# Optimization experiments

Hardware: AMD Instinct MI355X
Metric: run time of the kernel (lower is better)

The kernel has to match this reference:

```python
import jax, jax.numpy as jnp
import numpy as np

B, H, W = 4, 256, 256
TARGET_BETA0 = 5
TARGET_LIFETIME = 0.5
LOSS_SCALE = 100.0


def setup_inputs() -> dict:
    key = jax.random.key(0)
    k1, k2 = jax.random.split(key)
    prob_map = jax.random.uniform(k1, (B, 1, H, W), dtype=jnp.float32)
    roi_mask = (jax.random.uniform(k2, (B, 1, H, W)) < 0.9).astype(jnp.float32)
    return {"prob_map": prob_map, "roi_mask": roi_mask}


def _ph0_topk_loss(f):
    """0-dim persistent homology (V-filtration, 4-connectivity) of f:[H,W],
    then standard top-k MSE(target_lifetime) loss. Equivalent to
    cripser.compute_ph_torch(f, maxdim=0, filtration='V') + _standard_loss.
    Algorithm: Kruskal over grid edges with weight max(f[u],f[v]), elder rule.
    All combinatorics run on stop_gradient values; births/deaths are
    differentiable gathers from f at the paired pixel indices."""
    Hh, Ww = f.shape
    N = Hh * Ww
    fv = f.reshape(-1)
    fvc = jax.lax.stop_gradient(fv)

    idx2d = jnp.arange(N, dtype=jnp.int32).reshape(Hh, Ww)
    r_u = idx2d[:, :-1].reshape(-1)  # right edges
    r_v = r_u + 1
    d_u = idx2d[:-1, :].reshape(-1)  # down edges
    d_v = d_u + Ww
    eu = jnp.concatenate([r_u, d_u])
    ev = jnp.concatenate([r_v, d_v])
    ew = jnp.maximum(fvc[eu], fvc[ev])
    order = jnp.argsort(ew)  # process edges by increasing filtration value
    eu, ev = eu[order], ev[order]

    parent0 = jnp.arange(N, dtype=jnp.int32)

    def step(parent, uv):
        u, v = uv[0], uv[1]

        def find(x):
            return jax.lax.while_loop(lambda y: parent[y] != y, lambda y: parent[y], x)

        ru = find(u)
        rv = find(v)
        merge = ru != rv
        # Invariant: a root is the argmin pixel of its component, so
        # fvc[root] is the component's birth value. Elder rule: the root
        # with smaller birth value survives (ties -> smaller index).
        older_u = (fvc[ru] < fvc[rv]) | ((fvc[ru] == fvc[rv]) & (ru < rv))
        keep = jnp.where(older_u, ru, rv)
        die = jnp.where(older_u, rv, ru)
        b_idx = jnp.where(merge, die, -1)  # birth pixel of the dying comp
        d_pix = jnp.where(fvc[u] >= fvc[v], u, v)  # death = max endpoint
        d_idx = jnp.where(merge, d_pix, -1)
        parent = parent.at[die].set(jnp.where(merge, keep, die))
        parent = parent.at[u].set(jnp.where(merge, keep, ru))  # path compression
        parent = parent.at[v].set(jnp.where(merge, keep, rv))
        return parent, (b_idx, d_idx)

    _, (pb, pd_) = jax.lax.scan(step, parent0, jnp.stack([eu, ev], axis=1))

    valid = pb >= 0
    births = fv[jnp.maximum(pb, 0)]
    deaths = fv[jnp.maximum(pd_, 0)]
    life = jnp.where(valid, deaths - births, 0.0)  # lifetimes >= 0

    # sort descending; invalid slots to the end (keys are stop-gradient)
    key_ = jnp.where(valid, jax.lax.stop_gradient(life), -jnp.inf)
    top = jnp.argsort(-key_)[:TARGET_BETA0]
    topk = life[top]
    vk = valid[top]
    n_use = jnp.sum(vk)  # = min(num_finite, target_beta0)
    sq = jnp.where(vk, (topk - TARGET_LIFETIME) ** 2, 0.0)
    return jnp.sum(sq) / jnp.maximum(n_use, 1).astype(f.dtype)


def reference(prob_map, roi_mask):
    prob = prob_map[:, 0] * roi_mask[:, 0]  # roi masking; (1-roi)*0 is a no-op
    filtration = 1.0 - prob
    losses = jax.vmap(_ph0_topk_loss)(filtration)
    return jnp.mean(losses) * LOSS_SCALE
```

## Files before the change

kernel.cpp:

```cpp
#include <hip/hip_runtime.h>
#include <stdint.h>

#define NPIX 65536
#define NRE  65280
#define NE   130560
#define NIMG 4
#define LTPB 1024
#define ETPB 1024
#define NBLK_L (NIMG*32)
#define TPIX 2048
#define EPAD 4096
#define KMAX 4096
#define HSZ  1024
#define LHSZ 2048
#define ECAP 4096
typedef unsigned long long u64;

__device__ __forceinline__ int ufind(unsigned* lbl, int x){
  int r = x, c = (int)lbl[r];
  while (c != r){ r = c; c = (int)lbl[r]; }
  while ((int)lbl[x] != r){ int n = (int)lbl[x]; lbl[x] = (unsigned)r; x = n; }
  return r;
}
__device__ __forceinline__ int ufind16(unsigned short* uf, int x){
  int r = x, c = (int)uf[r];
  while (c != r){ r = c; c = (int)uf[r]; }
  while ((int)uf[x] != r){ int n = (int)uf[x]; uf[x] = (unsigned short)r; x = n; }
  return r;
}

__device__ __forceinline__ void merge5(float* a, const float* b){
  float out[5]; int ia = 0, ib = 0;
  #pragma unroll
  for (int k = 0; k < 5; ++k){
    float av = (ia < 5) ? a[ia] : -2.0f;
    float bv = (ib < 5) ? b[ib] : -2.0f;
    if (av >= bv){ out[k] = av; ++ia; } else { out[k] = bv; ++ib; }
  }
  #pragma unroll
  for (int k = 0; k < 5; ++k) a[k] = out[k];
}

__device__ __forceinline__ void ins5(float* t5, float v){
  if (v > t5[4]){
    int j = 4;
    while (j > 0 && t5[j-1] < v){ t5[j] = t5[j-1]; --j; }
    t5[j] = v;
  }
}

__global__ __launch_bounds__(LTPB)
void ph0_local(const float* __restrict__ prob, const float* __restrict__ roi,
               float* __restrict__ Fg, float* __restrict__ LIFEg,
               unsigned* __restrict__ LBLg, u64* __restrict__ LAg,
               unsigned* __restrict__ C, unsigned* __restrict__ C2,
               unsigned* __restrict__ MAPg, unsigned* __restrict__ KGg,
               float* __restrict__ T5g)
{
  const int blk = blockIdx.x;
  const int img = blk >> 5;
  const int tile = blk & 31;
  const int tr = tile >> 2, tc = tile & 3;
  const int gr0 = tr*32, gc0 = tc*64;
  const int tid = threadIdx.x;
  const int lane = tid & 63;

  const float* pm = prob + img*NPIX;
  const float* rm = roi  + img*NPIX;
  float* F = Fg + img*NPIX;
  float* LIFE = LIFEg + img*NPIX;
  unsigned* LBL = LBLg + img*NPIX;
  unsigned* MAP = MAPg + img*NPIX;
  unsigned* KG  = KGg  + img*NPIX;
  u64* LA = LAg + (size_t)img*NE;

  __shared__ float          sf[TPIX];
  __shared__ unsigned       slbl[TPIX];
  __shared__ unsigned       smeb[2][TPIX];
  __shared__ unsigned short el[2][EPAD];
  __shared__ unsigned       aux[EPAD];
  __shared__ unsigned       bkw[192];
  __shared__ unsigned short bkp[192];
  __shared__ unsigned       s_fired[TPIX/32];
  __shared__ float          s_t5w[(LTPB/64)*5];
  __shared__ int s_n[3];

  float t5[5] = {-1.f,-1.f,-1.f,-1.f,-1.f};

  for (int p = tid; p < TPIX; p += LTPB){
    int gp = ((gr0 + (p>>6))<<8) + gc0 + (p&63);
    float fv = 1.0f - pm[gp]*rm[gp];
    sf[p] = fv; slbl[p] = (unsigned)p;
    smeb[0][p] = 0xFFFFFFFFu; smeb[1][p] = 0xFFFFFFFFu;
    F[gp] = fv; LIFE[gp] = 0.0f;
  }
  if (tid < 3) s_n[tid] = 0;
  if (tid < TPIX/32) s_fired[tid] = 0;
  for (int s = tid; s < 192; s += LTPB){
    unsigned wv = 0xFFFFFFFFu; int p = 0; int gq = -1;
    if (s < 32){ if (tc > 0){ p = s*64;        gq = ((gr0+s)<<8)    + gc0 - 1;  } }
    else if (s < 64){ int k=s-32;  if (tc < 3){ p = k*64+63;  gq = ((gr0+k)<<8)  + gc0 + 64; } }
    else if (s < 128){ int k=s-64; if (tr > 0){ p = k;        gq = ((gr0-1)<<8)  + gc0 + k;  } }
    else { int k=s-128;            if (tr < 7){ p = 31*64+k;  gq = ((gr0+32)<<8) + gc0 + k;  } }
    if (gq >= 0){
      int gp = ((gr0 + (p>>6))<<8) + gc0 + (p&63);
      float fp = 1.0f - pm[gp]*rm[gp];
      float fq = 1.0f - pm[gq]*rm[gq];
      wv = __float_as_uint(fmaxf(fp, fq));
    }
    bkw[s] = wv; bkp[s] = (unsigned short)p;
  }
  __syncthreads();

  int M = EPAD, cur = 0;
  for (int rd = 0; rd < 100000; ++rd){
    int nxt = cur ^ 1;
    unsigned* sme = smeb[rd & 1];
    if (tid < 192){
      unsigned wv = bkw[tid];
      if (wv != 0xFFFFFFFFu) atomicMin(&sme[ufind(slbl, (int)bkp[tid])], wv);
    }
    int Mpad = (M + 63) & ~63;
    for (int idx = tid; idx < Mpad; idx += LTPB){
      bool keep = false; int e=0,u=0,v=0,a=0,b=0;
      if (idx < M){
        e = (rd == 0) ? idx : (int)el[cur][idx];
        bool valid;
        if (e < 2048){ u=e; v=e+1; valid = ((e&63)!=63); }
        else { u=e-2048; v=u+64; valid = ((u>>6)!=31); }
        if (valid){
          a = ufind(slbl,u); b = ufind(slbl,v);
          if (a != b){
            unsigned wb = __float_as_uint(fmaxf(sf[u],sf[v]));
            atomicMin(&sme[a],wb); atomicMin(&sme[b],wb);
            keep = true;
          }
        }
      }
      u64 m = __ballot(keep);
      if (m){
        int pos0 = __popcll(m & ((1ULL<<lane)-1));
        int leader = __ffsll((long long)m)-1;
        int base = 0;
        if (lane == leader) base = atomicAdd(&s_n[rd%3], __popcll(m));
        base = __shfl(base, leader);
        if (keep){
          el[nxt][base+pos0] = (unsigned short)e;
          aux[base+pos0] = (unsigned)a | ((unsigned)b<<16);
        }
      }
    }
    __syncthreads();
    int n = s_n[rd%3];
    cur = nxt;
    if (n == M || n == 0){ M = n; break; }
    M = n;
    for (int idx = tid; idx < M; idx += LTPB){
      int e = (int)el[cur][idx];
      unsigned ab = aux[idx];
      int a = (int)(ab & 0xFFFFu), b = (int)(ab >> 16);
      int u, v;
      if (e < 2048){ u = e; v = e + 1; } else { u = e - 2048; v = u + 64; }
      float w = fmaxf(sf[u], sf[v]);
      unsigned wb = __float_as_uint(w);
      float fa = sf[a], fb = sf[b];
      bool bd = (fb < fa) || ((fb == fa) && (b < a));
      int die = bd ? a : b, keep = bd ? b : a;
      if (sme[die] == wb){
        slbl[die] = (unsigned)keep;
        int gd = ((gr0 + (die>>6))<<8) + gc0 + (die&63);
        float lt = w - (bd ? fa : fb);
        LIFE[gd] = lt;
        unsigned bbit = 1u << (die & 31);
        if (!(atomicOr(&s_fired[die >> 5], bbit) & bbit)) ins5(t5, lt);
      }
    }
    {
      unsigned* smeN = smeb[(rd+1) & 1];
      for (int i = tid; i < TPIX; i += LTPB) smeN[i] = 0xFFFFFFFFu;
      if (tid == 0) s_n[(rd+1)%3] = 0;
    }
    __syncthreads();
  }

  unsigned* posm = smeb[0];
  for (int p = tid; p < TPIX; p += LTPB){
    int r = ufind(slbl, p);
    int gp = ((gr0 + (p>>6))<<8) + gc0 + (p&63);
    LBL[gp] = (unsigned)(((gr0 + (r>>6))<<8) + gc0 + (r&63));
  }
  __syncthreads();
  for (int p = tid; p < TPIX; p += LTPB){
    if ((int)slbl[p] == p){
      unsigned pos = atomicAdd(&C2[img], 1u);
      posm[p] = pos;
      unsigned gp = (unsigned)(((gr0 + (p>>6))<<8) + gc0 + (p&63));
      MAP[gp] = pos;
      KG[pos] = gp;
    }
  }
  __syncthreads();

  unsigned* hk = (unsigned*)&el[cur ^ 1][0];
  unsigned* hw = slbl;
  for (int i = tid; i < LHSZ; i += LTPB){ hk[i] = 0xFFFFFFFFu; hw[i] = 0xFFFFFFFFu; }
  __syncthreads();

  unsigned* ctr = &C[img];
  int Mpad2 = (M + 63) & ~63;
  for (int idx = tid; idx < Mpad2; idx += LTPB){
    bool spill = false;
    u64 rec = 0;
    if (idx < M){
      int e = (int)el[cur][idx];
      unsigned ab = aux[idx];
      int a = (int)(ab & 0xFFFFu), b = (int)(ab >> 16);
      int u, v;
      if (e < 2048){ u = e; v = e + 1; } else { u = e - 2048; v = u + 64; }
      unsigned wb = __float_as_uint(fmaxf(sf[u], sf[v]));
      int lo = a < b ? a : b, hi = a < b ? b : a;
      unsigned key = ((unsigned)lo << 11) | (unsigned)hi;
      unsigned h = ((key * 2654435761u) >> 21) & (LHSZ-1);
      bool ins = false;
      #pragma unroll
      for (int t = 0; t < 8; ++t){
        unsigned old = atomicCAS(&hk[h], 0xFFFFFFFFu, key);
        if (old == 0xFFFFFFFFu || old == key){ atomicMin(&hw[h], wb); ins = true; break; }
        h = (h + 1) & (LHSZ-1);
      }
      if (!ins){
        spill = true;
        rec = ((u64)wb << 32) | ((u64)posm[a] << 16) | posm[b];
      }
    }
    u64 m = __ballot(spill);
    if (m){
      int pos0 = __popcll(m & ((1ULL<<lane)-1));
      int leader = __ffsll((long long)m)-1;
      unsigned base = 0;
      if (lane == leader) base = atomicAdd(ctr, (unsigned)__popcll(m));
      base = (unsigned)__shfl((int)base, leader);
      if (spill) LA[base + pos0] = rec;
    }
  }
  __syncthreads();
  for (int h = tid; h < LHSZ; h += LTPB){
    unsigned key = hk[h];
    bool ok = (key != 0xFFFFFFFFu);
    u64 rec = 0;
    if (ok){
      int a = (int)(key >> 11), b = (int)(key & 0x7FFu);
      rec = ((u64)hw[h] << 32) | ((u64)posm[a] << 16) | posm[b];
    }
    u64 m = __ballot(ok);
    if (m){
      int pos0 = __popcll(m & ((1ULL<<lane)-1));
      int leader = __ffsll((long long)m)-1;
      unsigned base = 0;
      if (lane == leader) base = atomicAdd(ctr, (unsigned)__popcll(m));
      base = (unsigned)__shfl((int)base, leader);
      if (ok) LA[base + pos0] = rec;
    }
  }

  #pragma unroll
  for (int off = 1; off < 64; off <<= 1){
    float o[5];
    #pragma unroll
    for (int k = 0; k < 5; ++k) o[k] = __shfl_xor(t5[k], off);
    merge5(t5, o);
  }
  if (lane == 0){
    int wv = tid >> 6;
    #pragma unroll
    for (int k = 0; k < 5; ++k) s_t5w[wv*5+k] = t5[k];
  }
  __syncthreads();
  if (tid < 64){
    float u5[5];
    #pragma unroll
    for (int k = 0; k < 5; ++k) u5[k] = (tid < LTPB/64) ? s_t5w[tid*5+k] : -2.0f;
    #pragma unroll
    for (int off = 1; off < 16; off <<= 1){
      float o[5];
      #pragma unroll
      for (int k = 0; k < 5; ++k) o[k] = __shfl_xor(u5[k], off);
      merge5(u5, o);
    }
    if (tid == 0){
      #pragma unroll
      for (int k = 0; k < 5; ++k) T5g[blk*5+k] = u5[k];
    }
  }
}

#define RUN_ROUNDS_GLOBAL(UF, ME, RNK)                                       \
  for (int k = tid; k < K; k += ETPB){                                       \
    unsigned g = kg[k];                                                      \
    UF[k] = (unsigned short)k;                                               \
    RNK[k] = ((u64)__float_as_uint(f[g]) << 32) | g;                         \
  }                                                                          \
  __syncthreads();                                                           \
  for (int rd = 0; rd < 70000 && n > 0; ++rd){                               \
    for (int k = tid; k < K; k += ETPB) ME[k] = 0xFFFFFFFFu;                 \
    if (tid == 0) s_n[0] = 0;                                                \
    __syncthreads();                                                         \
    int Mpad = (n + 63) & ~63;                                               \
    for (int idx = tid; idx < Mpad; idx += ETPB){                            \
      bool keep = false; unsigned wb = 0; int a = 0, b = 0;                  \
      if (idx < n){                                                          \
        u64 rec = src[idx];                                                  \
        wb = (unsigned)(rec >> 32);                                          \
        a = (int)((rec >> 16) & 0xFFFFu);                                    \
        b = (int)(rec & 0xFFFFu);                                            \
        a = ufind16(UF, a); b = ufind16(UF, b);                              \
        if (a != b){ atomicMin(&ME[a], wb); atomicMin(&ME[b], wb); keep = true; } \
      }                                                                      \
      u64 m = __ballot(keep);                                                \
      if (m){                                                                \
        int pos0 = __popcll(m & ((1ULL<<lane)-1));                           \
        int leader = __ffsll((long long)m)-1;                                \
        int base = 0;                                                        \
        if (lane == leader) base = atomicAdd(&s_n[0], __popcll(m));          \
        base = __shfl(base, leader);                                         \
        if (keep) dst[base+pos0] = ((u64)wb<<32)|((u64)(unsigned)a<<16)|(unsigned)b; \
      }                                                                      \
    }                                                                        \
    __syncthreads();                                                         \
    int nn = s_n[0];                                                         \
    for (int idx = tid; idx < nn; idx += ETPB){                              \
      u64 rec = dst[idx];                                                    \
      unsigned wb = (unsigned)(rec >> 32);                                   \
      int a = (int)((rec >> 16) & 0xFFFFu);                                  \
      int b = (int)(rec & 0xFFFFu);                                          \
      bool bd = RNK[b] < RNK[a];                                             \
      int die = bd ? a : b, kp = bd ? b : a;                                 \
      if (ME[die] == wb){                                                    \
        UF[die] = (unsigned short)kp;                                        \
        u64 rk = RNK[die];                                                   \
        life[(unsigned)(rk & 0xFFFFFFFFu)] =                                 \
            __uint_as_float(wb) - __uint_as_float((unsigned)(rk >> 32));     \
      }                                                                      \
    }                                                                        \
    __syncthreads();                                                         \
    u64* t = src; src = dst; dst = t; n = nn;                                \
  }

__global__ __launch_bounds__(ETPB)
void ph0_endgame(const float* __restrict__ Fg, float* __restrict__ LIFEg,
                 unsigned* __restrict__ LBLg, unsigned* __restrict__ MAPg,
                 unsigned* __restrict__ KGg, u64* __restrict__ LAg,
                 u64* __restrict__ LBg, u64* __restrict__ GRg,
                 const unsigned* __restrict__ C, const unsigned* __restrict__ C2,
                 const float* __restrict__ T5g,
                 float* __restrict__ LOSS, unsigned* __restrict__ DONE,
                 float* __restrict__ out)
{
  const int img = blockIdx.x, tid = threadIdx.x;
  const int lane = tid & 63;
  const float* f = Fg + img*NPIX;
  float* life = LIFEg + img*NPIX;
  unsigned* lblg = LBLg + img*NPIX;
  unsigned* map  = MAPg + img*NPIX;
  const unsigned* kg = KGg + img*NPIX;
  u64* src = LAg + (size_t)img*NE;
  u64* dst = LBg + (size_t)img*NE;
  u64* rnk = GRg + (size_t)img*NPIX;

  __shared__ unsigned short s_uf[KMAX];
  __shared__ unsigned s_meB[2*KMAX];
  __shared__ unsigned s_hkB[2*HSZ];
  __shared__ unsigned s_hwB[2*HSZ];
  __shared__ u64 s_rnk[KMAX];
  __shared__ u64 s_lstA[ECAP];
  __shared__ u64 s_lstB[ECAP];
  __shared__ unsigned s_fired[KMAX/32];
  __shared__ float s_w5[(ETPB/64)*5];
  __shared__ int s_n[3];

  const int K = (int)C2[img];
  const int nInt = (int)C[img];

  for (int s = tid; s < 2560; s += ETPB){
    int gu, gv;
    if (s < 768){ int ci = s >> 8, row = s & 255, col = 63 + (ci<<6); gu = (row<<8)+col; gv = gu+1; }
    else { int k = s - 768; int ri = k >> 8, colh = k & 255, gr = 31 + (ri<<5); gu = (gr<<8)+colh; gv = gu+256; }
    unsigned ia = map[lblg[gu]];
    unsigned ib = map[lblg[gv]];
    unsigned wb = __float_as_uint(fmaxf(f[gu], f[gv]));
    src[nInt + s] = ((u64)wb << 32) | ((u64)ia << 16) | ib;
  }
  if (tid < 3) s_n[tid] = 0;
  int n = nInt + 2560;

  float t5[5] = {-1.f,-1.f,-1.f,-1.f,-1.f};

  if (K <= KMAX){
    for (int k = tid; k < K; k += ETPB){
      unsigned g = kg[k];
      s_uf[k] = (unsigned short)k;
      s_rnk[k] = ((u64)__float_as_uint(f[g]) << 32) | g;
      s_meB[k] = 0xFFFFFFFFu;
    }
    for (int h = tid; h < HSZ; h += ETPB){ s_hkB[h] = 0xFFFFFFFFu; s_hwB[h] = 0xFFFFFFFFu; }
    if (tid < KMAX/32) s_fired[tid] = 0;
    if (tid < 32*5) ins5(t5, T5g[img*(32*5) + tid]);
    __syncthreads();

    u64 *lsrc = s_lstA, *ldst = s_lstB;
    bool sL = false;

    for (int rd = 0; rd < 70000; ++rd){
      const int bi = rd & 1;
      unsigned* me = s_meB + bi*KMAX;
      unsigned* hk = s_hkB + bi*HSZ;
      unsigned* hw = s_hwB + bi*HSZ;
      const bool useHash = (n > 1024);
      const bool dL = (n <= ECAP);
      int Mpad = (n + 63) & ~63;
      for (int idx = tid; idx < Mpad; idx += ETPB){
        bool app = false; unsigned wb = 0; int a = 0, b = 0;
        if (idx < n){
          u64 rec = sL ? lsrc[idx] : src[idx];
          a = (int)((rec >> 16) & 0xFFFFu);
          b = (int)(rec & 0xFFFFu);
          a = ufind16(s_uf, a); b = ufind16(s_uf, b);
          if (a != b){
            wb = (unsigned)(rec >> 32);
            if (useHash){
              int lo = a < b ? a : b, hi = a < b ? b : a;
              unsigned key = ((unsigned)lo << 12) | (unsigned)hi;
              unsigned h = ((key * 2654435761u) >> 20) & (HSZ-1);
              bool ins = false;
              #pragma unroll
              for (int t = 0; t < 8; ++t){
                unsigned old = atomicCAS(&hk[h], 0xFFFFFFFFu, key);
                if (old == 0xFFFFFFFFu || old == key){ atomicMin(&hw[h], wb); ins = true; break; }
                h = (h + 1) & (HSZ-1);
              }
              if (!ins){ atomicMin(&me[a], wb); atomicMin(&me[b], wb); app = true; }
            } else {
              atomicMin(&me[a], wb); atomicMin(&me[b], wb); app = true;
            }
          }
        }
        u64 m = __ballot(app);
        if (m){
          int pos0 = __popcll(m & ((1ULL<<lane)-1));
          int leader = __ffsll((long long)m)-1;
          int base = 0;
          if (lane == leader) base = atomicAdd(&s_n[rd%3], __popcll(m));
          base = __shfl(base, leader);
          if (app){
            u64 r = ((u64)wb<<32)|((u64)(unsigned)a<<16)|(unsigned)b;
            if (dL) ldst[base+pos0] = r; else dst[base+pos0] = r;
          }
        }
      }
      __syncthreads();
      if (useHash){
        for (int h = tid; h < HSZ; h += ETPB){
          unsigned key = hk[h];
          bool okk = (key != 0xFFFFFFFFu);
          unsigned wb = 0; int a = 0, b = 0;
          if (okk){
            a = (int)(key >> 12); b = (int)(key & 0xFFFu);
            wb = hw[h];
            atomicMin(&me[a], wb); atomicMin(&me[b], wb);
          }
          u64 m = __ballot(okk);
          if (m){
            int pos0 = __popcll(m & ((1ULL<<lane)-1));
            int leader = __ffsll((long long)m)-1;
            int base = 0;
            if (lane == leader) base = atomicAdd(&s_n[rd%3], __popcll(m));
            base = __shfl(base, leader);
            if (okk){
              u64 r = ((u64)wb<<32)|((u64)(unsigned)a<<16)|(unsigned)b;
              if (dL) ldst[base+pos0] = r; else dst[base+pos0] = r;
            }
          }
        }
        __syncthreads();
      }
      int nn = s_n[rd%3];
      if (nn == 0) break;
      for (int idx = tid; idx < nn; idx += ETPB){
        u64 rec = dL ? ldst[idx] : dst[idx];
        unsigned wb = (unsigned)(rec >> 32);
        int a = (int)((rec >> 16) & 0xFFFFu);
        int b = (int)(rec & 0xFFFFu);
        u64 ra = s_rnk[a], rb = s_rnk[b];
        bool bd = rb < ra;
        int die = bd ? a : b, kp = bd ? b : a;
        if (me[die] == wb){
          s_uf[die] = (unsigned short)kp;
          unsigned bbit = 1u << (die & 31);
          if (!(atomicOr(&s_fired[die >> 5], bbit) & bbit)){
            u64 rk = bd ? ra : rb;
            ins5(t5, __uint_as_float(wb) - __uint_as_float((unsigned)(rk >> 32)));
          }
        }
      }
      {
        unsigned* meN = s_meB + (bi^1)*KMAX;
        for (int k = tid; k < K; k += ETPB) meN[k] = 0xFFFFFFFFu;
        if (nn > 1024){
          unsigned* hkN = s_hkB + (bi^1)*HSZ;
          unsigned* hwN = s_hwB + (bi^1)*HSZ;
          for (int h = tid; h < HSZ; h += ETPB){ hkN[h] = 0xFFFFFFFFu; hwN[h] = 0xFFFFFFFFu; }
        }
        if (tid == 0) s_n[(rd+1)%3] = 0;
      }
      __syncthreads();
      { u64* t = src; src = dst; dst = t; }
      { u64* t = lsrc; lsrc = ldst; ldst = t; }
      sL = dL;
      n = nn;
    }
  } else {
    __syncthreads();
    unsigned short* g_uf = (unsigned short*)lblg;
    unsigned*       g_me = map;
    u64*            g_rnk = rnk;
    RUN_ROUNDS_GLOBAL(g_uf, g_me, g_rnk)
    for (int i = tid; i < NPIX; i += ETPB) ins5(t5, life[i]);
  }

  #pragma unroll
  for (int off = 1; off < 64; off <<= 1){
    float o[5];
    #pragma unroll
    for (int k = 0; k < 5; ++k) o[k] = __shfl_xor(t5[k], off);
    merge5(t5, o);
  }
  if (lane == 0){
    int wv = tid >> 6;
    #pragma unroll
    for (int k = 0; k < 5; ++k) s_w5[wv*5+k] = t5[k];
  }
  __syncthreads();
  if (tid < 64){
    float u5[5];
    #pragma unroll
    for (int k = 0; k < 5; ++k) u5[k] = (tid < ETPB/64) ? s_w5[tid*5+k] : -2.0f;
    #pragma unroll
    for (int off = 1; off < 16; off <<= 1){
      float o[5];
      #pragma unroll
      for (int k = 0; k < 5; ++k) o[k] = __shfl_xor(u5[k], off);
      merge5(u5, o);
    }
    if (tid == 0){
      float lsum = 0.0f;
      #pragma unroll
      for (int k = 0; k < 5; ++k){ float d = u5[k] - 0.5f; lsum += d*d; }
      atomicExch(&LOSS[img], lsum * 0.2f);
      __threadfence();
      unsigned prev = atomicAdd(DONE, 1u);
      if (prev == NIMG - 1){
        float s = 0.0f;
        #pragma unroll
        for (int i = 0; i < NIMG; ++i) s += atomicAdd(&LOSS[i], 0.0f);
        out[0] = s * 25.0f;
      }
    }
  }
}

extern "C" void kernel_launch(void* const* d_in, const int* in_sizes, int n_in,
                              void* d_out, int out_size, void* d_ws, size_t ws_size,
                              hipStream_t stream)
{
  const float* prob = (const float*)d_in[0];
  const float* roi  = (const float*)d_in[1];
  char* ws = (char*)d_ws;
  const size_t SZL = (size_t)4*NE*8;
  float*    F    = (float*)(ws);
  float*    LIFE = (float*)(ws + (1u<<20));
  unsigned* LBL  = (unsigned*)(ws + (2u<<20));
  unsigned* MAP  = (unsigned*)(ws + (3u<<20));
  unsigned* KG   = (unsigned*)(ws + (4u<<20));
  u64*      LA   = (u64*)(ws + (5u<<20));
  u64*      LB   = (u64*)(ws + (5u<<20) + SZL);
  u64*      GR   = (u64*)(ws + (5u<<20) + 2*SZL);
  unsigned* C    = (unsigned*)(ws + (5u<<20) + 2*SZL + (2u<<20));
  unsigned* C2   = C + 4;
  unsigned* DONE = C + 8;
  float*    LOSS = (float*)((char*)C + 64);
  float*    T5   = (float*)(ws + (5u<<20) + 2*SZL - 2560);
  float*    out  = (float*)d_out;

  hipMemsetAsync(C, 0, 64, stream);
  ph0_local<<<NBLK_L, LTPB, 0, stream>>>(prob, roi, F, LIFE, LBL, LA, C, C2, MAP, KG, T5);
  ph0_endgame<<<NIMG, ETPB, 0, stream>>>(F, LIFE, LBL, MAP, KG, LA, LB, GR, C, C2, T5, LOSS, DONE, out);
}
```

Measured before the change: 268.8 us.

## Precompute component ids, cut weights and ranks in local kernel; flatten union-find per round

The local tile kernel now writes a compact component id per pixel, the tile-boundary cut-edge weights and the per-component rank records directly. The endgame kernel therefore no longer does chained gathers through label, map, key and filtration arrays, and it builds the cut-edge list in shared memory. Lifetimes are kept in shared memory and written once at the end. Both kernels also add a pointer-flattening pass after each round to shorten later find chains, and edge lists can straddle shared and global storage based on position. The trade-off is an extra full pass over the labels every round.

```diff
diff --git a/kernel.cpp b/kernel.cpp
--- a/kernel.cpp
+++ b/kernel.cpp
@@ -14,6 +14,7 @@
 #define HSZ  1024
 #define LHSZ 2048
 #define ECAP 4096
+#define NCUT 2560
 typedef unsigned long long u64;
 
 __device__ __forceinline__ int ufind(unsigned* lbl, int x){
@@ -27,6 +28,20 @@
   while (c != r){ r = c; c = (int)uf[r]; }
   while ((int)uf[x] != r){ int n = (int)uf[x]; uf[x] = (unsigned short)r; x = n; }
   return r;
+}
+__device__ __forceinline__ void uflat(unsigned* lbl, int x){
+  int r = (int)lbl[x];
+  if (r == x) return;
+  int c = (int)lbl[r];
+  while (c != r){ r = c; c = (int)lbl[r]; }
+  lbl[x] = (unsigned)r;
+}
+__device__ __forceinline__ void uflat16(unsigned short* uf, int x){
+  int r = (int)uf[x];
+  if (r == x) return;
+  int c = (int)uf[r];
+  while (c != r){ r = c; c = (int)uf[r]; }
+  uf[x] = (unsigned short)r;
 }
 
 __device__ __forceinline__ void merge5(float* a, const float* b){
@@ -51,10 +66,10 @@
 
 __global__ __launch_bounds__(LTPB)
 void ph0_local(const float* __restrict__ prob, const float* __restrict__ roi,
-               float* __restrict__ Fg, float* __restrict__ LIFEg,
-               unsigned* __restrict__ LBLg, u64* __restrict__ LAg,
+               float* __restrict__ LIFEg, unsigned* __restrict__ CIDg,
+               u64* __restrict__ LAg,
                unsigned* __restrict__ C, unsigned* __restrict__ C2,
-               unsigned* __restrict__ MAPg, unsigned* __restrict__ KGg,
+               unsigned* __restrict__ CUTWg, u64* __restrict__ RNKIg,
                float* __restrict__ T5g)
 {
   const int blk = blockIdx.x;
@@ -67,16 +82,16 @@
 
   const float* pm = prob + img*NPIX;
   const float* rm = roi  + img*NPIX;
-  float* F = Fg + img*NPIX;
   float* LIFE = LIFEg + img*NPIX;
-  unsigned* LBL = LBLg + img*NPIX;
-  unsigned* MAP = MAPg + img*NPIX;
-  unsigned* KG  = KGg  + img*NPIX;
+  unsigned* CID = CIDg + img*NPIX;
+  unsigned* CUTW = CUTWg + img*NCUT;
+  u64* RNKI = RNKIg + (size_t)img*NPIX;
   u64* LA = LAg + (size_t)img*NE;
 
   __shared__ float          sf[TPIX];
   __shared__ unsigned       slbl[TPIX];
   __shared__ unsigned       smeb[2][TPIX];
+  __shared__ float          slife[TPIX];
   __shared__ unsigned short el[2][EPAD];
   __shared__ unsigned       aux[EPAD];
   __shared__ unsigned       bkw[192];
@@ -92,7 +107,7 @@
     float fv = 1.0f - pm[gp]*rm[gp];
     sf[p] = fv; slbl[p] = (unsigned)p;
     smeb[0][p] = 0xFFFFFFFFu; smeb[1][p] = 0xFFFFFFFFu;
-    F[gp] = fv; LIFE[gp] = 0.0f;
+    slife[p] = 0.0f;
   }
   if (tid < 3) s_n[tid] = 0;
   if (tid < TPIX/32) s_fired[tid] = 0;
@@ -112,13 +127,20 @@
   }
   __syncthreads();
 
+  if (tid < 192){
+    int s = tid;
+    if (s >= 32 && s < 64  && tc < 3) CUTW[(tc<<8) | (gr0 + (s-32))] = bkw[s];
+    if (s >= 128           && tr < 7) CUTW[768 + (tr<<8) + (gc0 + (s-128))] = bkw[s];
+  }
+
   int M = EPAD, cur = 0;
   for (int rd = 0; rd < 100000; ++rd){
     int nxt = cur ^ 1;
     unsigned* sme = smeb[rd & 1];
-    if (tid < 192){
-      unsigned wv = bkw[tid];
-      if (wv != 0xFFFFFFFFu) atomicMin(&sme[ufind(slbl, (int)bkp[tid])], wv);
+    int bs = tid - (LTPB - 192);
+    if (bs >= 0){
+      unsigned wv = bkw[bs];
+      if (wv != 0xFFFFFFFFu) atomicMin(&sme[ufind(slbl, (int)bkp[bs])], wv);
     }
     int Mpad = (M + 63) & ~63;
     for (int idx = tid; idx < Mpad; idx += LTPB){
@@ -168,13 +190,13 @@
       int die = bd ? a : b, keep = bd ? b : a;
       if (sme[die] == wb){
         slbl[die] = (unsigned)keep;
-        int gd = ((gr0 + (die>>6))<<8) + gc0 + (die&63);
         float lt = w - (bd ? fa : fb);
-        LIFE[gd] = lt;
+        slife[die] = lt;
         unsigned bbit = 1u << (die & 31);
         if (!(atomicOr(&s_fired[die >> 5], bbit) & bbit)) ins5(t5, lt);
       }
     }
+    for (int p = tid; p < TPIX; p += LTPB) uflat(slbl, p);
     {
       unsigned* smeN = smeb[(rd+1) & 1];
       for (int i = tid; i < TPIX; i += LTPB) smeN[i] = 0xFFFFFFFFu;
@@ -184,20 +206,20 @@
   }
 
   unsigned* posm = smeb[0];
-  for (int p = tid; p < TPIX; p += LTPB){
-    int r = ufind(slbl, p);
-    int gp = ((gr0 + (p>>6))<<8) + gc0 + (p&63);
-    LBL[gp] = (unsigned)(((gr0 + (r>>6))<<8) + gc0 + (r&63));
-  }
-  __syncthreads();
   for (int p = tid; p < TPIX; p += LTPB){
     if ((int)slbl[p] == p){
       unsigned pos = atomicAdd(&C2[img], 1u);
       posm[p] = pos;
       unsigned gp = (unsigned)(((gr0 + (p>>6))<<8) + gc0 + (p&63));
-      MAP[gp] = pos;
-      KG[pos] = gp;
-    }
+      RNKI[pos] = ((u64)__float_as_uint(sf[p]) << 32) | gp;
+    }
+  }
+  __syncthreads();
+  for (int p = tid; p < TPIX; p += LTPB){
+    int r = ufind(slbl, p);
+    int gp = ((gr0 + (p>>6))<<8) + gc0 + (p&63);
+    CID[gp] = posm[r];
+    LIFE[gp] = slife[p];
   }
   __syncthreads();
 
@@ -295,11 +317,7 @@
 }
 
 #define RUN_ROUNDS_GLOBAL(UF, ME, RNK)                                       \
-  for (int k = tid; k < K; k += ETPB){                                       \
-    unsigned g = kg[k];                                                      \
-    UF[k] = (unsigned short)k;                                               \
-    RNK[k] = ((u64)__float_as_uint(f[g]) << 32) | g;                         \
-  }                                                                          \
+  for (int k = tid; k < K; k += ETPB) UF[k] = (unsigned short)k;             \
   __syncthreads();                                                           \
   for (int rd = 0; rd < 70000 && n > 0; ++rd){                               \
     for (int k = tid; k < K; k += ETPB) ME[k] = 0xFFFFFFFFu;                 \
@@ -347,10 +365,9 @@
   }
 
 __global__ __launch_bounds__(ETPB)
-void ph0_endgame(const float* __restrict__ Fg, float* __restrict__ LIFEg,
-                 unsigned* __restrict__ LBLg, unsigned* __restrict__ MAPg,
-                 unsigned* __restrict__ KGg, u64* __restrict__ LAg,
-                 u64* __restrict__ LBg, u64* __restrict__ GRg,
+void ph0_endgame(float* __restrict__ LIFEg, unsigned* __restrict__ CIDg,
+                 const unsigned* __restrict__ CUTWg, u64* __restrict__ RNKIg,
+                 u64* __restrict__ LAg, u64* __restrict__ LBg,
                  const unsigned* __restrict__ C, const unsigned* __restrict__ C2,
                  const float* __restrict__ T5g,
                  float* __restrict__ LOSS, unsigned* __restrict__ DONE,
@@ -358,14 +375,12 @@
 {
   const int img = blockIdx.x, tid = threadIdx.x;
   const int lane = tid & 63;
-  const float* f = Fg + img*NPIX;
   float* life = LIFEg + img*NPIX;
-  unsigned* lblg = LBLg + img*NPIX;
-  unsigned* map  = MAPg + img*NPIX;
-  const unsigned* kg = KGg + img*NPIX;
+  unsigned* cid = CIDg + img*NPIX;
+  const unsigned* cw = CUTWg + img*NCUT;
+  u64* RNKI = RNKIg + (size_t)img*NPIX;
   u64* src = LAg + (size_t)img*NE;
   u64* dst = LBg + (size_t)img*NE;
-  u64* rnk = GRg + (size_t)img*NPIX;
 
   __shared__ unsigned short s_uf[KMAX];
   __shared__ unsigned s_meB[2*KMAX];
@@ -381,25 +396,24 @@
   const int K = (int)C2[img];
   const int nInt = (int)C[img];
 
-  for (int s = tid; s < 2560; s += ETPB){
+  for (int s = tid; s < NCUT; s += ETPB){
     int gu, gv;
     if (s < 768){ int ci = s >> 8, row = s & 255, col = 63 + (ci<<6); gu = (row<<8)+col; gv = gu+1; }
     else { int k = s - 768; int ri = k >> 8, colh = k & 255, gr = 31 + (ri<<5); gu = (gr<<8)+colh; gv = gu+256; }
-    unsigned ia = map[lblg[gu]];
-    unsigned ib = map[lblg[gv]];
-    unsigned wb = __float_as_uint(fmaxf(f[gu], f[gv]));
-    src[nInt + s] = ((u64)wb << 32) | ((u64)ia << 16) | ib;
+    unsigned ia = cid[gu];
+    unsigned ib = cid[gv];
+    unsigned wb = cw[s];
+    s_lstA[s] = ((u64)wb << 32) | ((u64)ia << 16) | ib;
   }
   if (tid < 3) s_n[tid] = 0;
-  int n = nInt + 2560;
+  int n = nInt + NCUT;
 
   float t5[5] = {-1.f,-1.f,-1.f,-1.f,-1.f};
 
   if (K <= KMAX){
     for (int k = tid; k < K; k += ETPB){
-      unsigned g = kg[k];
       s_uf[k] = (unsigned short)k;
-      s_rnk[k] = ((u64)__float_as_uint(f[g]) << 32) | g;
+      s_rnk[k] = RNKI[k];
       s_meB[k] = 0xFFFFFFFFu;
     }
     for (int h = tid; h < HSZ; h += ETPB){ s_hkB[h] = 0xFFFFFFFFu; s_hwB[h] = 0xFFFFFFFFu; }
@@ -408,7 +422,6 @@
     __syncthreads();
 
     u64 *lsrc = s_lstA, *ldst = s_lstB;
-    bool sL = false;
 
     for (int rd = 0; rd < 70000; ++rd){
       const int bi = rd & 1;
@@ -416,12 +429,13 @@
       unsigned* hk = s_hkB + bi*HSZ;
       unsigned* hw = s_hwB + bi*HSZ;
       const bool useHash = (n > 1024);
-      const bool dL = (n <= ECAP);
       int Mpad = (n + 63) & ~63;
       for (int idx = tid; idx < Mpad; idx += ETPB){
         bool app = false; unsigned wb = 0; int a = 0, b = 0;
         if (idx < n){
-          u64 rec = sL ? lsrc[idx] : src[idx];
+          u64 rec;
+          if (rd == 0) rec = (idx < NCUT) ? lsrc[idx] : src[idx - NCUT];
+          else         rec = (idx < ECAP) ? lsrc[idx] : src[idx];
           a = (int)((rec >> 16) & 0xFFFFu);
           b = (int)(rec & 0xFFFFu);
           a = ufind16(s_uf, a); b = ufind16(s_uf, b);
@@ -453,7 +467,8 @@
           base = __shfl(base, leader);
           if (app){
             u64 r = ((u64)wb<<32)|((u64)(unsigned)a<<16)|(unsigned)b;
-            if (dL) ldst[base+pos0] = r; else dst[base+pos0] = r;
+            int pos = base+pos0;
+            if (pos < ECAP) ldst[pos] = r; else dst[pos] = r;
           }
         }
       }
@@ -477,7 +492,8 @@
             base = __shfl(base, leader);
             if (okk){
               u64 r = ((u64)wb<<32)|((u64)(unsigned)a<<16)|(unsigned)b;
-              if (dL) ldst[base+pos0] = r; else dst[base+pos0] = r;
+              int pos = base+pos0;
+              if (pos < ECAP) ldst[pos] = r; else dst[pos] = r;
             }
           }
         }
@@ -486,7 +502,7 @@
       int nn = s_n[rd%3];
       if (nn == 0) break;
       for (int idx = tid; idx < nn; idx += ETPB){
-        u64 rec = dL ? ldst[idx] : dst[idx];
+        u64 rec = (idx < ECAP) ? ldst[idx] : dst[idx];
         unsigned wb = (unsigned)(rec >> 32);
         int a = (int)((rec >> 16) & 0xFFFFu);
         int b = (int)(rec & 0xFFFFu);
@@ -502,6 +518,7 @@
           }
         }
       }
+      for (int k = tid; k < K; k += ETPB) uflat16(s_uf, k);
       {
         unsigned* meN = s_meB + (bi^1)*KMAX;
         for (int k = tid; k < K; k += ETPB) meN[k] = 0xFFFFFFFFu;
@@ -515,14 +532,15 @@
       __syncthreads();
       { u64* t = src; src = dst; dst = t; }
       { u64* t = lsrc; lsrc = ldst; ldst = t; }
-      sL = dL;
       n = nn;
     }
   } else {
     __syncthreads();
-    unsigned short* g_uf = (unsigned short*)lblg;
-    unsigned*       g_me = map;
-    u64*            g_rnk = rnk;
+    for (int s = tid; s < NCUT; s += ETPB) src[nInt + s] = s_lstA[s];
+    __syncthreads();
+    unsigned short* g_uf = (unsigned short*)cid;
+    unsigned*       g_me = (unsigned*)(cid + NPIX/2);
+    u64*            g_rnk = RNKI;
     RUN_ROUNDS_GLOBAL(g_uf, g_me, g_rnk)
     for (int i = tid; i < NPIX; i += ETPB) ins5(t5, life[i]);
   }
@@ -576,14 +594,12 @@
   const float* roi  = (const float*)d_in[1];
   char* ws = (char*)d_ws;
   const size_t SZL = (size_t)4*NE*8;
-  float*    F    = (float*)(ws);
   float*    LIFE = (float*)(ws + (1u<<20));
-  unsigned* LBL  = (unsigned*)(ws + (2u<<20));
-  unsigned* MAP  = (unsigned*)(ws + (3u<<20));
-  unsigned* KG   = (unsigned*)(ws + (4u<<20));
+  unsigned* CID  = (unsigned*)(ws + (2u<<20));
+  unsigned* CUTW = (unsigned*)(ws + (3u<<20));
   u64*      LA   = (u64*)(ws + (5u<<20));
   u64*      LB   = (u64*)(ws + (5u<<20) + SZL);
-  u64*      GR   = (u64*)(ws + (5u<<20) + 2*SZL);
+  u64*      RNKI = (u64*)(ws + (5u<<20) + 2*SZL);
   unsigned* C    = (unsigned*)(ws + (5u<<20) + 2*SZL + (2u<<20));
   unsigned* C2   = C + 4;
   unsigned* DONE = C + 8;
@@ -592,6 +608,6 @@
   float*    out  = (float*)d_out;
 
   hipMemsetAsync(C, 0, 64, stream);
-  ph0_local<<<NBLK_L, LTPB, 0, stream>>>(prob, roi, F, LIFE, LBL, LA, C, C2, MAP, KG, T5);
-  ph0_endgame<<<NIMG, ETPB, 0, stream>>>(F, LIFE, LBL, MAP, KG, LA, LB, GR, C, C2, T5, LOSS, DONE, out);
-}
+  ph0_local<<<NBLK_L, LTPB, 0, stream>>>(prob, roi, LIFE, CID, LA, C, C2, CUTW, RNKI, T5);
+  ph0_endgame<<<NIMG, ETPB, 0, stream>>>(LIFE, CID, CUTW, RNKI, LA, LB, C, C2, T5, LOSS, DONE, out);
+}
```

New measurement: 262.4 us. 1.02x faster.
